# Kernel optimization log

Hardware: AMD Instinct MI355X
Metric: run time of the kernel (lower is better)

## Reference

```python
import jax, jax.numpy as jnp
import numpy as np
from jax import lax

HEADS = 4
SR = 4
LN_EPS = 1e-5


def setup_inputs() -> dict:
    key = jax.random.key(0)
    ks = jax.random.split(key, 8)
    B, N, C = 8, 4096, 256
    w_scale = 0.05  # keep attention logits in a sane range
    return {
        "x": jax.random.normal(ks[0], (B, N, C), jnp.float32),
        "h": 64,
        "w": 64,
        "Wq": jax.random.normal(ks[1], (C, C), jnp.float32) * w_scale,
        "Wkv": jax.random.normal(ks[2], (C, 2 * C), jnp.float32) * w_scale,
        "sr_w": jax.random.normal(ks[3], (C, C, SR, SR), jnp.float32) * w_scale,
        "sr_b": jnp.zeros((C,), jnp.float32),
        "ln_g": jnp.ones((C,), jnp.float32),
        "ln_b": jnp.zeros((C,), jnp.float32),
        "Wo": jax.random.normal(ks[4], (C, C), jnp.float32) * w_scale,
        "bo": jnp.zeros((C,), jnp.float32),
    }


def _layernorm(x, g, b):
    mu = x.mean(-1, keepdims=True)
    var = ((x - mu) ** 2).mean(-1, keepdims=True)
    return (x - mu) * lax.rsqrt(var + LN_EPS) * g + b


def reference(x, h, w, Wq, Wkv, sr_w, sr_b, ln_g, ln_b, Wo, bo):
    B, N, C = x.shape
    hd = C // HEADS
    scale = hd ** -0.5
    # Q projection -> [B, H, N, hd]
    q = (x @ Wq).reshape(B, N, HEADS, hd).transpose(0, 2, 1, 3)
    # spatial reduction of K/V tokens: strided conv + LayerNorm
    x_kv = x.transpose(0, 2, 1).reshape(B, C, h, w)  # b (h w) c -> b c h w
    x_kv = lax.conv_general_dilated(
        x_kv, sr_w, window_strides=(SR, SR), padding="VALID",
        dimension_numbers=("NCHW", "OIHW", "NCHW"))
    x_kv = x_kv + sr_b[None, :, None, None]
    Nk = (h // SR) * (w // SR)
    x_kv = x_kv.reshape(B, C, Nk).transpose(0, 2, 1)  # b c h w -> b (h w) c
    x_kv = _layernorm(x_kv, ln_g, ln_b)
    # KV projection -> k, v each [B, H, Nk, hd]
    kv = (x_kv @ Wkv).reshape(B, Nk, 2, HEADS, hd)
    k = kv[:, :, 0].transpose(0, 2, 1, 3)
    v = kv[:, :, 1].transpose(0, 2, 1, 3)
    # attention: full [B, H, N, Nk] score matrix, softmax over kv axis
    att = jax.nn.softmax(jnp.einsum("bhxd,bhyd->bhxy", q, k) * scale, axis=-1)
    out = jnp.einsum("bhxy,bhyd->bhxd", att, v)
    out = out.transpose(0, 2, 1, 3).reshape(B, N, C)  # b h l d -> b l (h d)
    return out @ Wo + bo
```

## Files before the change

kernel.cpp:

```cpp
#include <hip/hip_runtime.h>

typedef __bf16 bf16;
typedef bf16 bf16x8 __attribute__((ext_vector_type(8)));
typedef bf16 bf16x4 __attribute__((ext_vector_type(4)));
typedef float f32x4 __attribute__((ext_vector_type(4)));

#define MFMA16(a, b, c) __builtin_amdgcn_mfma_f32_16x16x32_bf16(a, b, c, 0, 0, 0)

__global__ void k_prep(const float* __restrict__ x, const float* __restrict__ Wq,
                       const float* __restrict__ Wkv, const float* __restrict__ Wo,
                       const float* __restrict__ srw,
                       bf16* __restrict__ x_bf, bf16* __restrict__ WqT,
                       bf16* __restrict__ WkvT, bf16* __restrict__ WoT,
                       bf16* __restrict__ srwT) {
  int bid = blockIdx.x, tid = threadIdx.x;
  if (bid < 8192) {
    int i = (bid * 256 + tid) * 4;
    float4 v = *(const float4*)(x + i);
    bf16x4 o;
    o[0] = (bf16)v.x; o[1] = (bf16)v.y; o[2] = (bf16)v.z; o[3] = (bf16)v.w;
    *(bf16x4*)(x_bf + i) = o;
  } else if (bid < 9216) {
    int id = (bid - 8192) * 256 + tid;
    if (id < 65536) {
      int c = id >> 8, r = id & 255;
      WqT[id] = (bf16)Wq[r * 256 + c];
    } else if (id < 196608) {
      int l = id - 65536;
      int c = l >> 8, r = l & 255;
      WkvT[l] = (bf16)Wkv[r * 512 + c];
    } else {
      int l = id - 196608;
      int c = l >> 8, r = l & 255;
      WoT[l] = (bf16)Wo[r * 256 + c];
    }
  } else {
    int id4 = ((bid - 9216) * 256 + tid) * 4;
    int o = id4 >> 12, rem = id4 & 4095;
    int i = rem >> 4, p = rem & 15;
    float4 v = *(const float4*)(srw + id4);
    srwT[(o << 12) + ((p + 0) << 8) + i] = (bf16)v.x;
    srwT[(o << 12) + ((p + 1) << 8) + i] = (bf16)v.y;
    srwT[(o << 12) + ((p + 2) << 8) + i] = (bf16)v.z;
    srwT[(o << 12) + ((p + 3) << 8) + i] = (bf16)v.w;
  }
}

template <int AMODE, int EMODE>
__global__ __launch_bounds__(256, 2) void k_gemm(
    const bf16* __restrict__ A, const bf16* __restrict__ Bt,
    void* __restrict__ Cout, const float* __restrict__ bias,
    int M, int N, int K) {
  constexpr int LDT = 72;
  __shared__ alignas(16) bf16 As[64 * LDT];
  __shared__ alignas(16) bf16 Bs[64 * LDT];
  int tid = threadIdx.x;
  int m0 = blockIdx.x * 64, n0 = blockIdx.y * 64;
  int kbeg = blockIdx.z * K;
  int wave = tid >> 6, lane = tid & 63;
  int quad = lane >> 4, l16 = lane & 15;

  f32x4 acc[4];
#pragma unroll
  for (int i = 0; i < 4; i++) acc[i] = (f32x4){0.f, 0.f, 0.f, 0.f};

  for (int k0 = kbeg; k0 < kbeg + K; k0 += 64) {
#pragma unroll
    for (int t = 0; t < 2; t++) {
      int c = tid + t * 256;
      int row = c >> 3, c8 = (c & 7) * 8;
      const bf16* asrc;
      if constexpr (AMODE == 0) {
        asrc = A + (size_t)(m0 + row) * K + k0 + c8;
      } else {
        int m = m0 + row;
        int b = m >> 8, tt = m & 255;
        int oh = tt >> 4, ow = tt & 15;
        int p = k0 >> 8;
        int kh = p >> 2, kw = p & 3;
        int tok = (oh * 4 + kh) * 64 + ow * 4 + kw;
        asrc = A + ((size_t)(b * 4096 + tok) << 8) + (k0 & 255) + c8;
      }
      *(bf16x8*)&As[row * LDT + c8] = *(const bf16x8*)asrc;
      *(bf16x8*)&Bs[row * LDT + c8] =
          *(const bf16x8*)(Bt + (size_t)(n0 + row) * ((AMODE == 1) ? 4096 : K) + k0 + c8);
    }
    __syncthreads();
#pragma unroll
    for (int kk = 0; kk < 64; kk += 32) {
      bf16x8 af = *(const bf16x8*)&As[(wave * 16 + l16) * LDT + kk + quad * 8];
#pragma unroll
      for (int nt = 0; nt < 4; nt++) {
        bf16x8 bfr = *(const bf16x8*)&Bs[(nt * 16 + l16) * LDT + kk + quad * 8];
        acc[nt] = MFMA16(af, bfr, acc[nt]);
      }
    }
    __syncthreads();
  }

  int rbase = m0 + wave * 16 + quad * 4;
#pragma unroll
  for (int nt = 0; nt < 4; nt++) {
    int col = n0 + nt * 16 + l16;
#pragma unroll
    for (int r = 0; r < 4; r++) {
      float v = acc[nt][r];
      int row = rbase + r;
      if constexpr (EMODE == 2) {
        int b = row >> 8, key = row & 255;
        int isv = col >> 8, c2 = col & 255;
        int hh = c2 >> 6, d = c2 & 63;
        int bh = b * 4 + hh;
        bf16* dst = (bf16*)Cout;
        if (isv == 0)
          dst[(((size_t)bh) * 256 + key) * 64 + d] = (bf16)v;
        else
          dst[32 * 256 * 64 + (((size_t)bh) * 64 + d) * 256 + key] = (bf16)v;
      } else if constexpr (EMODE == 3) {
        ((float*)Cout)[(size_t)row * N + col] = v + bias[col];
      } else {
        ((float*)Cout)[((size_t)blockIdx.z * M + row) * N + col] = v;
      }
    }
  }
}

__global__ void k_ln(const float* __restrict__ part, const float* __restrict__ srb,
                     const float* __restrict__ g, const float* __restrict__ bb,
                     bf16* __restrict__ out) {
  int row = blockIdx.x * 4 + (threadIdx.x >> 6);
  int lane = threadIdx.x & 63;
  size_t off = (size_t)row * 256 + lane * 4;
  float4 v = *(const float4*)&part[off];
#pragma unroll
  for (int z = 1; z < 8; z++) {
    float4 p = *(const float4*)&part[(size_t)z * 2048 * 256 + off];
    v.x += p.x; v.y += p.y; v.z += p.z; v.w += p.w;
  }
  int c = lane * 4;
  v.x += srb[c + 0]; v.y += srb[c + 1]; v.z += srb[c + 2]; v.w += srb[c + 3];
  float s = v.x + v.y + v.z + v.w;
#pragma unroll
  for (int i = 1; i < 64; i <<= 1) s += __shfl_xor(s, i, 64);
  float mu = s * (1.f / 256.f);
  float d0 = v.x - mu, d1 = v.y - mu, d2 = v.z - mu, d3 = v.w - mu;
  float q = d0 * d0 + d1 * d1 + d2 * d2 + d3 * d3;
#pragma unroll
  for (int i = 1; i < 64; i <<= 1) q += __shfl_xor(q, i, 64);
  float rs = rsqrtf(q * (1.f / 256.f) + 1e-5f);
  bf16x4 o;
  o[0] = (bf16)(d0 * rs * g[c + 0] + bb[c + 0]);
  o[1] = (bf16)(d1 * rs * g[c + 1] + bb[c + 1]);
  o[2] = (bf16)(d2 * rs * g[c + 2] + bb[c + 2]);
  o[3] = (bf16)(d3 * rs * g[c + 3] + bb[c + 3]);
  *(bf16x4*)&out[(size_t)row * 256 + c] = o;
}

__global__ __launch_bounds__(256, 2) void k_attn(
    const bf16* __restrict__ xbf,
    const bf16* __restrict__ WqT,
    const bf16* __restrict__ Kb,
    const bf16* __restrict__ Vt_g,
    bf16* __restrict__ O) {
  int bh = blockIdx.x, qt = blockIdx.y;
  int b = bh >> 2, h = bh & 3;
  int tid = threadIdx.x, wave = tid >> 6, lane = tid & 63;
  int quad = lane >> 4, l16 = lane & 15;

  __shared__ alignas(16) bf16 smem[39936];
  bf16* R1 = smem;
  bf16* R2 = smem + 18432;
  bf16* Qs = smem + 35328;

#pragma unroll
  for (int t = 0; t < 8; t++) {
    int c = tid + t * 256;
    int row = c >> 5, c8 = (c & 31) * 8;
    *(bf16x8*)&R1[row * 264 + c8] =
        *(const bf16x8*)&xbf[((size_t)(b * 4096 + qt * 64 + row) << 8) + c8];
    *(bf16x8*)&R2[row * 264 + c8] =
        *(const bf16x8*)&WqT[((size_t)(h * 64 + row) << 8) + c8];
  }
  __syncthreads();

  f32x4 q[4];
#pragma unroll
  for (int i = 0; i < 4; i++) q[i] = (f32x4){0.f, 0.f, 0.f, 0.f};
#pragma unroll
  for (int k0 = 0; k0 < 256; k0 += 32) {
    bf16x8 ax = *(const bf16x8*)&R1[(wave * 16 + l16) * 264 + k0 + quad * 8];
#pragma unroll
    for (int nt = 0; nt < 4; nt++) {
      bf16x8 bw = *(const bf16x8*)&R2[(nt * 16 + l16) * 264 + k0 + quad * 8];
      q[nt] = MFMA16(ax, bw, q[nt]);
    }
  }
  __syncthreads();

#pragma unroll
  for (int nt = 0; nt < 4; nt++)
#pragma unroll
    for (int r = 0; r < 4; r++)
      Qs[(wave * 16 + quad * 4 + r) * 72 + nt * 16 + l16] = (bf16)q[nt][r];

  const bf16* Kbh = Kb + (size_t)bh * 256 * 64;
#pragma unroll
  for (int t = 0; t < 8; t++) {
    int c = tid + t * 256;
    int row = c >> 3, c8 = (c & 7) * 8;
    *(bf16x8*)&R1[row * 72 + c8] = *(const bf16x8*)&Kbh[row * 64 + c8];
  }
  const bf16* Vbh = Vt_g + (size_t)bh * 64 * 256;
#pragma unroll
  for (int t = 0; t < 8; t++) {
    int c = tid + t * 256;
    int row = c >> 5, c8 = (c & 31) * 8;
    *(bf16x8*)&R2[row * 264 + c8] = *(const bf16x8*)&Vbh[row * 256 + c8];
  }
  __syncthreads();

  f32x4 s[16];
#pragma unroll
  for (int i = 0; i < 16; i++) s[i] = (f32x4){0.f, 0.f, 0.f, 0.f};
  bf16x8 aq0 = *(const bf16x8*)&Qs[(wave * 16 + l16) * 72 + 0 + quad * 8];
  bf16x8 aq1 = *(const bf16x8*)&Qs[(wave * 16 + l16) * 72 + 32 + quad * 8];
#pragma unroll
  for (int nt = 0; nt < 16; nt++) {
    bf16x8 b0 = *(const bf16x8*)&R1[(nt * 16 + l16) * 72 + 0 + quad * 8];
    bf16x8 b1 = *(const bf16x8*)&R1[(nt * 16 + l16) * 72 + 32 + quad * 8];
    s[nt] = MFMA16(aq0, b0, s[nt]);
    s[nt] = MFMA16(aq1, b1, s[nt]);
  }

  const float scale = 0.125f;
#pragma unroll
  for (int r = 0; r < 4; r++) {
    float m = -1e30f;
#pragma unroll
    for (int nt = 0; nt < 16; nt++) m = fmaxf(m, s[nt][r]);
#pragma unroll
    for (int i = 1; i < 16; i <<= 1) m = fmaxf(m, __shfl_xor(m, i, 64));
    float sum = 0.f;
#pragma unroll
    for (int nt = 0; nt < 16; nt++) {
      float e = __expf((s[nt][r] - m) * scale);
      s[nt][r] = e;
      sum += e;
    }
#pragma unroll
    for (int i = 1; i < 16; i <<= 1) sum += __shfl_xor(sum, i, 64);
    float inv = 1.f / sum;
#pragma unroll
    for (int nt = 0; nt < 16; nt++) s[nt][r] *= inv;
  }

  __syncthreads();
#pragma unroll
  for (int nt = 0; nt < 16; nt++)
#pragma unroll
    for (int r = 0; r < 4; r++)
      R1[(wave * 16 + quad * 4 + r) * 264 + nt * 16 + l16] = (bf16)s[nt][r];
  __syncthreads();

  f32x4 o[4];
#pragma unroll
  for (int i = 0; i < 4; i++) o[i] = (f32x4){0.f, 0.f, 0.f, 0.f};
#pragma unroll
  for (int k0 = 0; k0 < 256; k0 += 32) {
    bf16x8 ap = *(const bf16x8*)&R1[(wave * 16 + l16) * 264 + k0 + quad * 8];
#pragma unroll
    for (int nt = 0; nt < 4; nt++) {
      bf16x8 bv = *(const bf16x8*)&R2[(nt * 16 + l16) * 264 + k0 + quad * 8];
      o[nt] = MFMA16(ap, bv, o[nt]);
    }
  }

  size_t orow = (size_t)b * 4096 + qt * 64 + wave * 16 + quad * 4;
#pragma unroll
  for (int nt = 0; nt < 4; nt++) {
    int col = h * 64 + nt * 16 + l16;
#pragma unroll
    for (int r = 0; r < 4; r++) O[(orow + r) * 256 + col] = (bf16)o[nt][r];
  }
}

extern "C" void kernel_launch(void* const* d_in, const int* in_sizes, int n_in,
                              void* d_out, int out_size, void* d_ws, size_t ws_size,
                              hipStream_t stream) {
  (void)in_sizes; (void)n_in; (void)out_size; (void)ws_size;
  const float* x   = (const float*)d_in[0];
  const float* Wq  = (const float*)d_in[3];
  const float* Wkv = (const float*)d_in[4];
  const float* srw = (const float*)d_in[5];
  const float* srb = (const float*)d_in[6];
  const float* lng = (const float*)d_in[7];
  const float* lnb = (const float*)d_in[8];
  const float* Wo  = (const float*)d_in[9];
  const float* bo  = (const float*)d_in[10];
  float* out = (float*)d_out;

  char* ws = (char*)d_ws;
  bf16*  x_bf  = (bf16*)(ws + 0);
  bf16*  AObuf = (bf16*)(ws + 16777216);
  float* convp = (float*)(ws + 33554432);
  bf16*  WqT   = (bf16*)(ws + 50331648);
  bf16*  WkvT  = (bf16*)(ws + 50462720);
  bf16*  WoT   = (bf16*)(ws + 50724864);
  bf16*  srwT  = (bf16*)(ws + 50855936);
  bf16*  xln   = (bf16*)(ws + 52953088);
  bf16*  kvbuf = (bf16*)(ws + 54001664);

  k_prep<<<10240, 256, 0, stream>>>(x, Wq, Wkv, Wo, srw, x_bf, WqT, WkvT, WoT, srwT);
  k_gemm<1, 4><<<dim3(32, 4, 8), 256, 0, stream>>>(x_bf, srwT, convp, nullptr, 2048, 256, 512);
  k_ln<<<512, 256, 0, stream>>>(convp, srb, lng, lnb, xln);
  k_gemm<0, 2><<<dim3(32, 8), 256, 0, stream>>>(xln, WkvT, kvbuf, nullptr, 2048, 512, 256);
  k_attn<<<dim3(32, 64), 256, 0, stream>>>(x_bf, WqT, kvbuf, kvbuf + (size_t)32 * 256 * 64, AObuf);
  k_gemm<0, 3><<<dim3(512, 4), 256, 0, stream>>>(AObuf, WoT, out, bo, 32768, 256, 256);
}
```

Measured before the change: 186.8 us.

## Read attention operands directly from global and drop block-wide barriers

The attention kernel no longer stages x, Wq, K and V tiles in shared memory. It loads MFMA operands straight from global memory, so the data comes from cache. Shared memory now holds only each wave's private Q/P rows, and the __syncthreads barriers are replaced by a per-wave LDS waitcnt. The smaller LDS footprint lets the kernel request four blocks per CU instead of two. In exchange, operands are reloaded from global/L2 with a less coalesced access pattern, and the launch bound adds register pressure.

```diff
diff --git a/kernel.cpp b/kernel.cpp
--- a/kernel.cpp
+++ b/kernel.cpp
@@ -6,6 +6,7 @@
 typedef float f32x4 __attribute__((ext_vector_type(4)));
 
 #define MFMA16(a, b, c) __builtin_amdgcn_mfma_f32_16x16x32_bf16(a, b, c, 0, 0, 0)
+#define WAIT_LDS() __builtin_amdgcn_s_waitcnt(0xC07F)
 
 __global__ void k_prep(const float* __restrict__ x, const float* __restrict__ Wq,
                        const float* __restrict__ Wkv, const float* __restrict__ Wo,
@@ -156,78 +157,54 @@
   *(bf16x4*)&out[(size_t)row * 256 + c] = o;
 }
 
-__global__ __launch_bounds__(256, 2) void k_attn(
+__global__ __launch_bounds__(256, 4) void k_attn(
     const bf16* __restrict__ xbf,
     const bf16* __restrict__ WqT,
     const bf16* __restrict__ Kb,
     const bf16* __restrict__ Vt_g,
     bf16* __restrict__ O) {
+  constexpr int LDP = 264;
   int bh = blockIdx.x, qt = blockIdx.y;
   int b = bh >> 2, h = bh & 3;
   int tid = threadIdx.x, wave = tid >> 6, lane = tid & 63;
   int quad = lane >> 4, l16 = lane & 15;
 
-  __shared__ alignas(16) bf16 smem[39936];
-  bf16* R1 = smem;
-  bf16* R2 = smem + 18432;
-  bf16* Qs = smem + 35328;
-
-#pragma unroll
-  for (int t = 0; t < 8; t++) {
-    int c = tid + t * 256;
-    int row = c >> 5, c8 = (c & 31) * 8;
-    *(bf16x8*)&R1[row * 264 + c8] =
-        *(const bf16x8*)&xbf[((size_t)(b * 4096 + qt * 64 + row) << 8) + c8];
-    *(bf16x8*)&R2[row * 264 + c8] =
-        *(const bf16x8*)&WqT[((size_t)(h * 64 + row) << 8) + c8];
-  }
-  __syncthreads();
+  __shared__ alignas(16) bf16 Ps[64 * LDP];
+
+  const bf16* xrow  = xbf + ((size_t)(b * 4096 + qt * 64 + wave * 16 + l16) << 8) + quad * 8;
+  const bf16* wqrow = WqT + ((size_t)(h * 64) << 8);
+  const bf16* Kbh   = Kb + (size_t)bh * 256 * 64;
+  const bf16* Vbh   = Vt_g + (size_t)bh * 64 * 256;
 
   f32x4 q[4];
 #pragma unroll
   for (int i = 0; i < 4; i++) q[i] = (f32x4){0.f, 0.f, 0.f, 0.f};
 #pragma unroll
   for (int k0 = 0; k0 < 256; k0 += 32) {
-    bf16x8 ax = *(const bf16x8*)&R1[(wave * 16 + l16) * 264 + k0 + quad * 8];
+    bf16x8 ax = *(const bf16x8*)(xrow + k0);
 #pragma unroll
     for (int nt = 0; nt < 4; nt++) {
-      bf16x8 bw = *(const bf16x8*)&R2[(nt * 16 + l16) * 264 + k0 + quad * 8];
+      bf16x8 bw = *(const bf16x8*)&wqrow[((size_t)(nt * 16 + l16) << 8) + k0 + quad * 8];
       q[nt] = MFMA16(ax, bw, q[nt]);
     }
   }
-  __syncthreads();
 
 #pragma unroll
   for (int nt = 0; nt < 4; nt++)
 #pragma unroll
     for (int r = 0; r < 4; r++)
-      Qs[(wave * 16 + quad * 4 + r) * 72 + nt * 16 + l16] = (bf16)q[nt][r];
-
-  const bf16* Kbh = Kb + (size_t)bh * 256 * 64;
-#pragma unroll
-  for (int t = 0; t < 8; t++) {
-    int c = tid + t * 256;
-    int row = c >> 3, c8 = (c & 7) * 8;
-    *(bf16x8*)&R1[row * 72 + c8] = *(const bf16x8*)&Kbh[row * 64 + c8];
-  }
-  const bf16* Vbh = Vt_g + (size_t)bh * 64 * 256;
-#pragma unroll
-  for (int t = 0; t < 8; t++) {
-    int c = tid + t * 256;
-    int row = c >> 5, c8 = (c & 31) * 8;
-    *(bf16x8*)&R2[row * 264 + c8] = *(const bf16x8*)&Vbh[row * 256 + c8];
-  }
-  __syncthreads();
+      Ps[(wave * 16 + quad * 4 + r) * LDP + nt * 16 + l16] = (bf16)q[nt][r];
+  WAIT_LDS();
+  bf16x8 aq0 = *(const bf16x8*)&Ps[(wave * 16 + l16) * LDP + 0 + quad * 8];
+  bf16x8 aq1 = *(const bf16x8*)&Ps[(wave * 16 + l16) * LDP + 32 + quad * 8];
 
   f32x4 s[16];
 #pragma unroll
   for (int i = 0; i < 16; i++) s[i] = (f32x4){0.f, 0.f, 0.f, 0.f};
-  bf16x8 aq0 = *(const bf16x8*)&Qs[(wave * 16 + l16) * 72 + 0 + quad * 8];
-  bf16x8 aq1 = *(const bf16x8*)&Qs[(wave * 16 + l16) * 72 + 32 + quad * 8];
 #pragma unroll
   for (int nt = 0; nt < 16; nt++) {
-    bf16x8 b0 = *(const bf16x8*)&R1[(nt * 16 + l16) * 72 + 0 + quad * 8];
-    bf16x8 b1 = *(const bf16x8*)&R1[(nt * 16 + l16) * 72 + 32 + quad * 8];
+    bf16x8 b0 = *(const bf16x8*)&Kbh[(nt * 16 + l16) * 64 + 0 + quad * 8];
+    bf16x8 b1 = *(const bf16x8*)&Kbh[(nt * 16 + l16) * 64 + 32 + quad * 8];
     s[nt] = MFMA16(aq0, b0, s[nt]);
     s[nt] = MFMA16(aq1, b1, s[nt]);
   }
@@ -254,23 +231,22 @@
     for (int nt = 0; nt < 16; nt++) s[nt][r] *= inv;
   }
 
-  __syncthreads();
 #pragma unroll
   for (int nt = 0; nt < 16; nt++)
 #pragma unroll
     for (int r = 0; r < 4; r++)
-      R1[(wave * 16 + quad * 4 + r) * 264 + nt * 16 + l16] = (bf16)s[nt][r];
-  __syncthreads();
+      Ps[(wave * 16 + quad * 4 + r) * LDP + nt * 16 + l16] = (bf16)s[nt][r];
+  WAIT_LDS();
 
   f32x4 o[4];
 #pragma unroll
   for (int i = 0; i < 4; i++) o[i] = (f32x4){0.f, 0.f, 0.f, 0.f};
 #pragma unroll
   for (int k0 = 0; k0 < 256; k0 += 32) {
-    bf16x8 ap = *(const bf16x8*)&R1[(wave * 16 + l16) * 264 + k0 + quad * 8];
+    bf16x8 ap = *(const bf16x8*)&Ps[(wave * 16 + l16) * LDP + k0 + quad * 8];
 #pragma unroll
     for (int nt = 0; nt < 4; nt++) {
-      bf16x8 bv = *(const bf16x8*)&R2[(nt * 16 + l16) * 264 + k0 + quad * 8];
+      bf16x8 bv = *(const bf16x8*)&Vbh[(nt * 16 + l16) * 256 + k0 + quad * 8];
       o[nt] = MFMA16(ap, bv, o[nt]);
     }
   }
```

Result: slower. 243.1 us (+30.1%).
